# Kernel tuning notes

Measured on AMD Instinct MI355X. Metric: run time of the kernel, lower is better.

Reference implementation:

```python
import jax, jax.numpy as jnp
import numpy as np

N_NODES = 50000
N_EDGES = 800000
IN_DIM = 128
HID = 64
HEADS = 4
OUT_DIM = 20
NUM_GRAPHS = 64
NEG_SLOPE = 0.2  # PyG GATConv default leaky_relu slope


def _xavier(key, shape):
    fan_in, fan_out = shape[-1], shape[0]
    lim = float(np.sqrt(6.0 / (fan_in + fan_out)))
    return jax.random.uniform(key, shape, jnp.float32, -lim, lim)


def setup_inputs() -> dict:
    key = jax.random.key(0)
    ks = jax.random.split(key, 12)
    x = jax.random.normal(ks[0], (N_NODES, IN_DIM), jnp.float32)
    edge_index = jax.random.randint(ks[1], (2, N_EDGES), 0, N_NODES, jnp.int32)
    batch = jnp.sort(jax.random.randint(ks[2], (N_NODES,), 0, NUM_GRAPHS, jnp.int32))
    return {
        "x": x,
        "edge_index": edge_index,
        "batch": batch,
        # conv1: in -> HEADS*HID, concat
        "W1": _xavier(ks[3], (HEADS * HID, IN_DIM)),
        "a_src1": _xavier(ks[4], (HEADS, HID)),
        "a_dst1": _xavier(ks[5], (HEADS, HID)),
        "b1": jnp.zeros((HEADS * HID,), jnp.float32),
        # conv2: HEADS*HID -> HID, 1 head
        "W2": _xavier(ks[6], (HID, HEADS * HID)),
        "a_src2": _xavier(ks[7], (1, HID)),
        "a_dst2": _xavier(ks[8], (1, HID)),
        "b2": jnp.zeros((HID,), jnp.float32),
        "fc_W": _xavier(ks[9], (OUT_DIM, HID)),
        "fc_b": jnp.zeros((OUT_DIM,), jnp.float32),
    }


def _gat_conv(x, src, dst, W, a_src, a_dst, b, heads):
    """PyG GATConv: linear -> per-edge LeakyReLU attention -> softmax over
    incoming edges of each target node -> weighted scatter-sum. Self-loops
    are already included in (src, dst). Dropout omitted (eval mode)."""
    n = x.shape[0]
    h = (x @ W.T).reshape(n, heads, -1)            # [N, H, C]
    alpha_s = jnp.einsum("nhc,hc->nh", h, a_src)   # [N, H]
    alpha_d = jnp.einsum("nhc,hc->nh", h, a_dst)
    e = jax.nn.leaky_relu(alpha_s[src] + alpha_d[dst], NEG_SLOPE)  # [E, H]
    # numerically stable segment softmax over dst
    e_max = jax.ops.segment_max(e, dst, num_segments=n)
    e = jnp.exp(e - e_max[dst])
    denom = jax.ops.segment_sum(e, dst, num_segments=n)
    alpha = e / (denom[dst] + 1e-16)               # [E, H]
    msg = h[src] * alpha[..., None]                # [E, H, C]
    out = jax.ops.segment_sum(msg, dst, num_segments=n)  # [N, H, C]
    return out.reshape(n, -1) + b                  # concat heads


def reference(x, edge_index, batch, W1, a_src1, a_dst1, b1,
              W2, a_src2, a_dst2, b2, fc_W, fc_b):
    n = x.shape[0]
    loops = jnp.arange(n, dtype=edge_index.dtype)
    src = jnp.concatenate([edge_index[0], loops])  # add self-loops (PyG default)
    dst = jnp.concatenate([edge_index[1], loops])
    h = jax.nn.elu(_gat_conv(x, src, dst, W1, a_src1, a_dst1, b1, HEADS))
    h = jax.nn.elu(_gat_conv(h, src, dst, W2, a_src2, a_dst2, b2, 1))
    pooled = jax.ops.segment_max(h, batch, num_segments=NUM_GRAPHS)  # [G, HID]
    return pooled @ fc_W.T + fc_b                  # [G, OUT_DIM]
```

## Files before the change

### kernel.cpp

```cpp
#include <hip/hip_runtime.h>
#include <hip/hip_bf16.h>

#define N_NODES_C 50000
#define N_EDGES_C 800000
#define IN_DIM_C  128
#define HID_C     64
#define HEADS_C   4
#define OUT_DIM_C 20
#define NUM_GRAPHS_C 64
#define NEG_SLOPE 0.2f
#define SCAN_BLOCKS 196

typedef __attribute__((ext_vector_type(8))) short bf16x8;
typedef __attribute__((ext_vector_type(4))) float f32x4;
typedef __attribute__((ext_vector_type(2))) float f32x2;

__device__ __forceinline__ float lrelu(float t){ return t > 0.f ? t : NEG_SLOPE*t; }
__device__ __forceinline__ float elu1(float t){ return t > 0.f ? t : __expf(t)-1.f; }
__device__ __forceinline__ ushort f2bf(float f){
  unsigned u = __float_as_uint(f);
  return (ushort)((u + 0x7fffu + ((u>>16)&1u)) >> 16);
}
__device__ __forceinline__ float bflo(unsigned u){ return __uint_as_float(u<<16); }
__device__ __forceinline__ float bfhi(unsigned u){ return __uint_as_float(u & 0xffff0000u); }
__device__ __forceinline__ float bfs(ushort u){ return __uint_as_float(((unsigned)u)<<16); }

__global__ void hist_kernel(const int* __restrict__ ei, int* __restrict__ cursor){
  int e = blockIdx.x*256 + threadIdx.x;
  if (e < N_EDGES_C) atomicAdd(&cursor[ei[N_EDGES_C + e]], 1);
}

__global__ __launch_bounds__(256) void reduce_counts(const int* __restrict__ cursor, int* __restrict__ blockSums){
  int i = blockIdx.x*256 + threadIdx.x;
  int c = (i < N_NODES_C) ? cursor[i] : 0;
  #pragma unroll
  for(int d=32; d>=1; d>>=1) c += __shfl_xor(c, d);
  __shared__ int s4[4];
  int lane = threadIdx.x & 63, wv = threadIdx.x >> 6;
  if(lane==0) s4[wv] = c;
  __syncthreads();
  if(threadIdx.x==0) blockSums[blockIdx.x] = s4[0]+s4[1]+s4[2]+s4[3];
}

__global__ __launch_bounds__(256) void scan_sums(int* __restrict__ blockSums){
  __shared__ int sh[256];
  int t = threadIdx.x;
  int v = (t < SCAN_BLOCKS) ? blockSums[t] : 0;
  sh[t] = v; __syncthreads();
  #pragma unroll
  for(int off=1; off<256; off<<=1){
    int u = (t>=off) ? sh[t-off] : 0;
    __syncthreads();
    sh[t] += u;
    __syncthreads();
  }
  if(t < SCAN_BLOCKS) blockSums[t] = sh[t] - v;
}

__global__ __launch_bounds__(256) void scan_block(int* __restrict__ cursor, const int* __restrict__ blockSums,
                                                  int* __restrict__ offsets){
  __shared__ int sh[256];
  int t = threadIdx.x;
  int i = blockIdx.x*256 + t;
  int c = (i < N_NODES_C) ? cursor[i] : 0;
  sh[t] = c; __syncthreads();
  #pragma unroll
  for(int off=1; off<256; off<<=1){
    int u = (t>=off) ? sh[t-off] : 0;
    __syncthreads();
    sh[t] += u;
    __syncthreads();
  }
  int excl = sh[t] - c;
  int pref = blockSums[blockIdx.x] + excl;
  if(i < N_NODES_C){
    offsets[i] = pref;
    cursor[i]  = pref;
    if(i == N_NODES_C-1) offsets[N_NODES_C] = pref + c;
  }
}

__global__ void fill_kernel(const int* __restrict__ ei, int* __restrict__ cursor,
                            int* __restrict__ adj, int* __restrict__ dstOf){
  int e = blockIdx.x*256 + threadIdx.x;
  if (e >= N_EDGES_C) return;
  int sI = ei[e]; int d = ei[N_EDGES_C + e];
  int p = atomicAdd(&cursor[d], 1);
  adj[p] = sI;
  dstOf[p] = d;
}

__global__ __launch_bounds__(256) void wperm_kernel(const float* __restrict__ W1, const float* __restrict__ W2,
    ushort* __restrict__ Wp1h, ushort* __restrict__ Wp1l,
    ushort* __restrict__ Wp2h, ushort* __restrict__ Wp2l){
  int i = blockIdx.x*256 + threadIdx.x;
  const float* src; ushort *dh, *dl; int gidx;
  if(i < 4096){
    int kc = i>>10, oc = (i>>6)&15, l = i&63;
    src = W1 + (size_t)(oc*16 + (l&15))*IN_DIM_C + kc*32 + (l>>4)*8;
    dh = Wp1h; dl = Wp1l; gidx = i;
  } else if(i < 4096+2048){
    int i2 = i - 4096;
    int kc = i2>>8, oc = (i2>>6)&3, l = i2&63;
    src = W2 + (size_t)(oc*16 + (l&15))*256 + kc*32 + (l>>4)*8;
    dh = Wp2h; dl = Wp2l; gidx = i2;
  } else return;
  ushort h8[8], l8[8];
  #pragma unroll
  for(int j=0;j<8;j++){
    float f = src[j];
    ushort h = f2bf(f);
    h8[j] = h; l8[j] = f2bf(f - bfs(h));
  }
  #pragma unroll
  for(int j=0;j<8;j++){ dh[gidx*8+j] = h8[j]; dl[gidx*8+j] = l8[j]; }
}

#define HS1_STRIDE 260
__global__ __launch_bounds__(256) void lin1_mfma(const float* __restrict__ x,
    const ushort* __restrict__ Wp1h, const ushort* __restrict__ Wp1l,
    const float* __restrict__ aS, const float* __restrict__ aD,
    ushort* __restrict__ h1, float* __restrict__ as1, float* __restrict__ ad1){
  __shared__ ushort hs[64*HS1_STRIDE];
  int t = threadIdx.x, w = t>>6, l = t&63;
  int n0b = blockIdx.x*64;
  int n0 = n0b + w*16;
  bool active = (n0 < N_NODES_C);
  int row = l & 15, kg = l >> 4;
  if(active){
    bf16x8 ah[4], al[4];
    int gn = n0 + row; if(gn > N_NODES_C-1) gn = N_NODES_C-1;
    const float* xrow = x + (size_t)gn*IN_DIM_C + kg*8;
    #pragma unroll
    for(int kc=0;kc<4;kc++){
      float4 f0 = *(const float4*)(xrow + kc*32);
      float4 f1 = *(const float4*)(xrow + kc*32 + 4);
      float fv[8] = {f0.x,f0.y,f0.z,f0.w,f1.x,f1.y,f1.z,f1.w};
      #pragma unroll
      for(int j=0;j<8;j++){
        ushort h = f2bf(fv[j]);
        float r = fv[j] - bfs(h);
        ah[kc][j] = (short)h;
        al[kc][j] = (short)f2bf(r);
      }
    }
    const bf16x8* Wh = (const bf16x8*)Wp1h + l;
    const bf16x8* Wl = (const bf16x8*)Wp1l + l;
    f32x4 acc[16];
    #pragma unroll
    for(int oc=0;oc<16;oc++){
      f32x4 a = {0.f,0.f,0.f,0.f};
      const bf16x8* ph = Wh + oc*64;
      const bf16x8* pl = Wl + oc*64;
      #pragma unroll
      for(int kc=0;kc<4;kc++){
        bf16x8 bh = ph[kc*1024];
        bf16x8 bl = pl[kc*1024];
        a = __builtin_amdgcn_mfma_f32_16x16x32_bf16(ah[kc], bh, a, 0, 0, 0);
        a = __builtin_amdgcn_mfma_f32_16x16x32_bf16(ah[kc], bl, a, 0, 0, 0);
        a = __builtin_amdgcn_mfma_f32_16x16x32_bf16(al[kc], bh, a, 0, 0, 0);
      }
      acc[oc] = a;
    }
    #pragma unroll
    for(int h=0;h<4;h++){
      float ps0=0.f,ps1=0.f,ps2=0.f,ps3=0.f, pd0=0.f,pd1=0.f,pd2=0.f,pd3=0.f;
      #pragma unroll
      for(int oi=0;oi<4;oi++){
        int oc = h*4 + oi;
        float as_ = aS[oc*16 + row];
        float ad_ = aD[oc*16 + row];
        ps0 = fmaf(acc[oc][0], as_, ps0); pd0 = fmaf(acc[oc][0], ad_, pd0);
        ps1 = fmaf(acc[oc][1], as_, ps1); pd1 = fmaf(acc[oc][1], ad_, pd1);
        ps2 = fmaf(acc[oc][2], as_, ps2); pd2 = fmaf(acc[oc][2], ad_, pd2);
        ps3 = fmaf(acc[oc][3], as_, ps3); pd3 = fmaf(acc[oc][3], ad_, pd3);
      }
      #pragma unroll
      for(int d=1; d<16; d<<=1){
        ps0 += __shfl_xor(ps0,d); ps1 += __shfl_xor(ps1,d);
        ps2 += __shfl_xor(ps2,d); ps3 += __shfl_xor(ps3,d);
        pd0 += __shfl_xor(pd0,d); pd1 += __shfl_xor(pd1,d);
        pd2 += __shfl_xor(pd2,d); pd3 += __shfl_xor(pd3,d);
      }
      if(row==0){
        int nb4 = (n0 + kg*4)*4 + h;
        as1[nb4+0] = ps0; as1[nb4+4] = ps1; as1[nb4+8] = ps2; as1[nb4+12] = ps3;
        ad1[nb4+0] = pd0; ad1[nb4+4] = pd1; ad1[nb4+8] = pd2; ad1[nb4+12] = pd3;
      }
    }
    #pragma unroll
    for(int oc=0;oc<16;oc++){
      #pragma unroll
      for(int r=0;r<4;r++){
        hs[(w*16 + kg*4 + r)*HS1_STRIDE + oc*16 + row] = f2bf(acc[oc][r]);
      }
    }
  }
  __syncthreads();
  int nvalid = N_NODES_C - n0b; if(nvalid > 64) nvalid = 64;
  for(int i=t; i<nvalid*32; i+=256){
    int r = i>>5, c = i&31;
    ((uint4*)(h1 + (size_t)(n0b+r)*256))[c] = *(const uint4*)(hs + r*HS1_STRIDE + c*8);
  }
}

__global__ __launch_bounds__(256) void wexp1_kernel(const int* __restrict__ adj, const int* __restrict__ dstOf,
    const float* __restrict__ as1, const float* __restrict__ ad1, float* __restrict__ wExp){
  int i = blockIdx.x*256 + threadIdx.x;
  if(i >= N_EDGES_C) return;
  int s = adj[i], d = dstOf[i];
  float4 a = ((const float4*)as1)[s];
  float4 b = ((const float4*)ad1)[d];
  float4 w;
  w.x = __expf(lrelu(a.x+b.x));
  w.y = __expf(lrelu(a.y+b.y));
  w.z = __expf(lrelu(a.z+b.z));
  w.w = __expf(lrelu(a.w+b.w));
  ((float4*)wExp)[i] = w;
}

__global__ __launch_bounds__(256) void agg1_kernel(const int* __restrict__ offsets, const int* __restrict__ adj,
    const float* __restrict__ wExp, const ushort* __restrict__ h1,
    const float* __restrict__ as1, const float* __restrict__ ad1,
    const float* __restrict__ b1, float* __restrict__ out1){
  int wv = threadIdx.x>>6, lane = threadIdx.x&63;
  int v = blockIdx.x*4 + wv;
  int head = lane>>4;
  int start = offsets[v], end = offsets[v+1];
  float adh = ad1[(v<<2)+head];
  float ash = as1[(v<<2)+head];
  float wself = __expf(lrelu(ash+adh));
  float denom = wself;
  const char* hb = (const char*)h1;
  unsigned loff = ((unsigned)lane)<<3;
  uint2 pv = *(const uint2*)(hb + ((((unsigned)v)<<9) + loff));
  f32x2 acc01 = {wself*bflo(pv.x), wself*bfhi(pv.x)};
  f32x2 acc23 = {wself*bflo(pv.y), wself*bfhi(pv.y)};
  int i = start;
  for(; i+4 <= end; i += 4){
    int s0 = adj[i], s1 = adj[i+1], s2 = adj[i+2], s3 = adj[i+3];
    float w0 = wExp[(i<<2)+head];
    float w1 = wExp[((i+1)<<2)+head];
    float w2 = wExp[((i+2)<<2)+head];
    float w3 = wExp[((i+3)<<2)+head];
    uint2 p0 = *(const uint2*)(hb + ((((unsigned)s0)<<9) + loff));
    uint2 p1 = *(const uint2*)(hb + ((((unsigned)s1)<<9) + loff));
    uint2 p2 = *(const uint2*)(hb + ((((unsigned)s2)<<9) + loff));
    uint2 p3 = *(const uint2*)(hb + ((((unsigned)s3)<<9) + loff));
    denom += (w0+w1)+(w2+w3);
    f32x2 W0 = {w0,w0}, W1_ = {w1,w1}, W2_ = {w2,w2}, W3_ = {w3,w3};
    f32x2 h0a = {bflo(p0.x), bfhi(p0.x)}, h0b = {bflo(p0.y), bfhi(p0.y)};
    f32x2 h1a = {bflo(p1.x), bfhi(p1.x)}, h1b = {bflo(p1.y), bfhi(p1.y)};
    f32x2 h2a = {bflo(p2.x), bfhi(p2.x)}, h2b = {bflo(p2.y), bfhi(p2.y)};
    f32x2 h3a = {bflo(p3.x), bfhi(p3.x)}, h3b = {bflo(p3.y), bfhi(p3.y)};
    acc01 = __builtin_elementwise_fma(W0, h0a, acc01);
    acc23 = __builtin_elementwise_fma(W0, h0b, acc23);
    acc01 = __builtin_elementwise_fma(W1_, h1a, acc01);
    acc23 = __builtin_elementwise_fma(W1_, h1b, acc23);
    acc01 = __builtin_elementwise_fma(W2_, h2a, acc01);
    acc23 = __builtin_elementwise_fma(W2_, h2b, acc23);
    acc01 = __builtin_elementwise_fma(W3_, h3a, acc01);
    acc23 = __builtin_elementwise_fma(W3_, h3b, acc23);
  }
  for(; i < end; i++){
    int s0 = adj[i];
    float w0 = wExp[(i<<2)+head];
    uint2 p0 = *(const uint2*)(hb + ((((unsigned)s0)<<9) + loff));
    denom += w0;
    f32x2 W0 = {w0,w0};
    f32x2 h0a = {bflo(p0.x), bfhi(p0.x)}, h0b = {bflo(p0.y), bfhi(p0.y)};
    acc01 = __builtin_elementwise_fma(W0, h0a, acc01);
    acc23 = __builtin_elementwise_fma(W0, h0b, acc23);
  }
  float inv = 1.f/(denom + 1e-16f);
  float4 bv = *(const float4*)(b1 + (lane<<2));
  float4 r;
  r.x = elu1(acc01.x*inv + bv.x);
  r.y = elu1(acc01.y*inv + bv.y);
  r.z = elu1(acc23.x*inv + bv.z);
  r.w = elu1(acc23.y*inv + bv.w);
  *(float4*)(out1 + ((size_t)v<<8) + (lane<<2)) = r;
}

#define HS2_STRIDE 68
__global__ __launch_bounds__(256) void lin2_mfma(const float* __restrict__ in,
    const ushort* __restrict__ Wp2h, const ushort* __restrict__ Wp2l,
    const float* __restrict__ aS, const float* __restrict__ aD,
    ushort* __restrict__ h2, float* __restrict__ as2, float* __restrict__ ad2){
  __shared__ ushort hs[64*HS2_STRIDE];
  int t = threadIdx.x, w = t>>6, l = t&63;
  int n0b = blockIdx.x*64;
  int n0 = n0b + w*16;
  bool active = (n0 < N_NODES_C);
  int row = l & 15, kg = l >> 4;
  if(active){
    bf16x8 ah[8], al[8];
    int gn = n0 + row; if(gn > N_NODES_C-1) gn = N_NODES_C-1;
    const float* xrow = in + (size_t)gn*256 + kg*8;
    #pragma unroll
    for(int kc=0;kc<8;kc++){
      float4 f0 = *(const float4*)(xrow + kc*32);
      float4 f1 = *(const float4*)(xrow + kc*32 + 4);
      float fv[8] = {f0.x,f0.y,f0.z,f0.w,f1.x,f1.y,f1.z,f1.w};
      #pragma unroll
      for(int j=0;j<8;j++){
        ushort h = f2bf(fv[j]);
        float r = fv[j] - bfs(h);
        ah[kc][j] = (short)h;
        al[kc][j] = (short)f2bf(r);
      }
    }
    const bf16x8* Wh = (const bf16x8*)Wp2h + l;
    const bf16x8* Wl = (const bf16x8*)Wp2l + l;
    f32x4 acc[4];
    #pragma unroll
    for(int oc=0;oc<4;oc++){
      f32x4 a = {0.f,0.f,0.f,0.f};
      const bf16x8* ph = Wh + oc*64;
      const bf16x8* pl = Wl + oc*64;
      #pragma unroll
      for(int kc=0;kc<8;kc++){
        bf16x8 bh = ph[kc*256];
        bf16x8 bl = pl[kc*256];
        a = __builtin_amdgcn_mfma_f32_16x16x32_bf16(ah[kc], bh, a, 0, 0, 0);
        a = __builtin_amdgcn_mfma_f32_16x16x32_bf16(ah[kc], bl, a, 0, 0, 0);
        a = __builtin_amdgcn_mfma_f32_16x16x32_bf16(al[kc], bh, a, 0, 0, 0);
      }
      acc[oc] = a;
    }
    {
      float ps0=0.f,ps1=0.f,ps2=0.f,ps3=0.f, pd0=0.f,pd1=0.f,pd2=0.f,pd3=0.f;
      #pragma unroll
      for(int oc=0;oc<4;oc++){
        float as_ = aS[oc*16 + row];
        float ad_ = aD[oc*16 + row];
        ps0 = fmaf(acc[oc][0], as_, ps0); pd0 = fmaf(acc[oc][0], ad_, pd0);
        ps1 = fmaf(acc[oc][1], as_, ps1); pd1 = fmaf(acc[oc][1], ad_, pd1);
        ps2 = fmaf(acc[oc][2], as_, ps2); pd2 = fmaf(acc[oc][2], ad_, pd2);
        ps3 = fmaf(acc[oc][3], as_, ps3); pd3 = fmaf(acc[oc][3], ad_, pd3);
      }
      #pragma unroll
      for(int d=1; d<16; d<<=1){
        ps0 += __shfl_xor(ps0,d); ps1 += __shfl_xor(ps1,d);
        ps2 += __shfl_xor(ps2,d); ps3 += __shfl_xor(ps3,d);
        pd0 += __shfl_xor(pd0,d); pd1 += __shfl_xor(pd1,d);
        pd2 += __shfl_xor(pd2,d); pd3 += __shfl_xor(pd3,d);
      }
      if(row==0){
        int n = n0 + kg*4;
        as2[n+0] = ps0; as2[n+1] = ps1; as2[n+2] = ps2; as2[n+3] = ps3;
        ad2[n+0] = pd0; ad2[n+1] = pd1; ad2[n+2] = pd2; ad2[n+3] = pd3;
      }
    }
    #pragma unroll
    for(int oc=0;oc<4;oc++){
      #pragma unroll
      for(int r=0;r<4;r++){
        hs[(w*16 + kg*4 + r)*HS2_STRIDE + oc*16 + row] = f2bf(acc[oc][r]);
      }
    }
  }
  __syncthreads();
  int nvalid = N_NODES_C - n0b; if(nvalid > 64) nvalid = 64;
  for(int i=t; i<nvalid*8; i+=256){
    int r = i>>3, c = i&7;
    ((uint4*)(h2 + (size_t)(n0b+r)*64))[c] = *(const uint4*)(hs + r*HS2_STRIDE + c*8);
  }
}

__global__ __launch_bounds__(256) void wexp2_kernel(const int* __restrict__ adj, const int* __restrict__ dstOf,
    const float* __restrict__ as2, const float* __restrict__ ad2, float* __restrict__ wExp2){
  int i = blockIdx.x*256 + threadIdx.x;
  if(i >= N_EDGES_C) return;
  int s = adj[i], d = dstOf[i];
  wExp2[i] = __expf(lrelu(as2[s] + ad2[d]));
}

__global__ __launch_bounds__(256) void agg2_kernel(const int* __restrict__ offsets, const int* __restrict__ adj,
    const float* __restrict__ wExp2, const ushort* __restrict__ h2,
    const float* __restrict__ as2, const float* __restrict__ ad2,
    const float* __restrict__ b2, float* __restrict__ out2){
  int wv = threadIdx.x>>6, lane = threadIdx.x&63;
  int v = blockIdx.x*4 + wv;
  int half = lane>>5, sl = lane&31;
  int start = offsets[v], end = offsets[v+1];
  float adv = ad2[v], asv = as2[v];
  float wself = __expf(lrelu(asv+adv));
  const unsigned* hu = (const unsigned*)h2;
  float denom = half ? 0.f : wself;
  f32x2 acc = {0.f, 0.f};
  if(!half){
    unsigned us = hu[(((unsigned)v)<<5) + sl];
    acc.x = wself*bflo(us); acc.y = wself*bfhi(us);
  }
  for(int i=start+half; i<end; i+=2){
    int s = adj[i];
    float wg = wExp2[i];
    unsigned u = hu[(((unsigned)s)<<5) + sl];
    denom += wg;
    f32x2 Wp = {wg, wg};
    f32x2 hp = {bflo(u), bfhi(u)};
    acc = __builtin_elementwise_fma(Wp, hp, acc);
  }
  acc.x += __shfl_xor(acc.x, 32);
  acc.y += __shfl_xor(acc.y, 32);
  denom += __shfl_xor(denom, 32);
  if(!half){
    float inv = 1.f/(denom + 1e-16f);
    float2 bv = *(const float2*)(b2 + sl*2);
    float2 r;
    r.x = elu1(acc.x*inv + bv.x);
    r.y = elu1(acc.y*inv + bv.y);
    *(float2*)(out2 + (((size_t)v)<<6) + sl*2) = r;
  }
}

__global__ __launch_bounds__(256) void pool_fc_kernel(const float* __restrict__ out2, const int* __restrict__ batch,
    const float* __restrict__ fcW, const float* __restrict__ fcb, float* __restrict__ out){
  int g = blockIdx.x;
  int tid=threadIdx.x; int c = tid&63; int slot = tid>>6;
  int lo=0, hi=N_NODES_C;
  while(lo<hi){ int mid=(lo+hi)>>1; if(batch[mid] < g) lo=mid+1; else hi=mid; }
  int start=lo;
  hi=N_NODES_C;
  while(lo<hi){ int mid=(lo+hi)>>1; if(batch[mid] < g+1) lo=mid+1; else hi=mid; }
  int end=lo;
  float mm = -INFINITY;
  #pragma unroll 4
  for(int n=start+slot; n<end; n+=4) mm = fmaxf(mm, out2[(size_t)n*64+c]);
  __shared__ float sred[4][64];
  sred[slot][c]=mm;
  __syncthreads();
  if(tid < 64){
    float p = fmaxf(fmaxf(sred[0][tid],sred[1][tid]), fmaxf(sred[2][tid],sred[3][tid]));
    sred[0][tid]=p;
  }
  __syncthreads();
  if(tid < OUT_DIM_C){
    float acc = fcb[tid];
    #pragma unroll
    for(int cc=0;cc<64;cc++) acc = fmaf(sred[0][cc], fcW[tid*64+cc], acc);
    out[g*OUT_DIM_C + tid] = acc;
  }
}

extern "C" void kernel_launch(void* const* d_in, const int* in_sizes, int n_in,
                              void* d_out, int out_size, void* d_ws, size_t ws_size,
                              hipStream_t stream) {
  const float* x   = (const float*)d_in[0];
  const int*   ei  = (const int*)  d_in[1];
  const int*   bat = (const int*)  d_in[2];
  const float* W1  = (const float*)d_in[3];
  const float* aS1 = (const float*)d_in[4];
  const float* aD1 = (const float*)d_in[5];
  const float* b1  = (const float*)d_in[6];
  const float* W2  = (const float*)d_in[7];
  const float* aS2 = (const float*)d_in[8];
  const float* aD2 = (const float*)d_in[9];
  const float* b2  = (const float*)d_in[10];
  const float* fcW = (const float*)d_in[11];
  const float* fcb = (const float*)d_in[12];
  float* out = (float*)d_out;

  char* w = (char*)d_ws;
  size_t off = 0;
  auto alloc = [&](size_t bytes)->char* {
    char* p = w + off; off = (off + bytes + 255) & ~(size_t)255; return p;
  };
  int* offsets   = (int*)alloc((N_NODES_C+1)*sizeof(int));
  int* cursor    = (int*)alloc((size_t)N_NODES_C*sizeof(int));
  int* blockSums = (int*)alloc(SCAN_BLOCKS*sizeof(int));
  int* adj       = (int*)alloc((size_t)(N_EDGES_C+4)*sizeof(int));
  int* dstOf     = (int*)alloc((size_t)N_EDGES_C*sizeof(int));
  ushort* Wp1h   = (ushort*)alloc((size_t)4096*8*sizeof(ushort));
  ushort* Wp1l   = (ushort*)alloc((size_t)4096*8*sizeof(ushort));
  ushort* Wp2h   = (ushort*)alloc((size_t)2048*8*sizeof(ushort));
  ushort* Wp2l   = (ushort*)alloc((size_t)2048*8*sizeof(ushort));
  ushort* h1     = (ushort*)alloc((size_t)N_NODES_C*256*sizeof(ushort));
  float* as1     = (float*)alloc((size_t)N_NODES_C*4*sizeof(float));
  float* ad1     = (float*)alloc((size_t)N_NODES_C*4*sizeof(float));
  float* out1    = (float*)alloc((size_t)N_NODES_C*256*sizeof(float));
  float* wExp    = (float*)alloc(((size_t)N_EDGES_C*4+4)*sizeof(float));
  ushort* h2  = h1;
  float* as2  = as1;
  float* ad2  = ad1;
  float* out2 = out1;
  float* wExp2 = wExp;
  (void)ws_size; (void)in_sizes; (void)n_in; (void)out_size;

  hipMemsetAsync(cursor, 0, (size_t)N_NODES_C*sizeof(int), stream);
  hist_kernel<<<(N_EDGES_C+255)/256, 256, 0, stream>>>(ei, cursor);
  reduce_counts<<<SCAN_BLOCKS, 256, 0, stream>>>(cursor, blockSums);
  scan_sums<<<1, 256, 0, stream>>>(blockSums);
  scan_block<<<SCAN_BLOCKS, 256, 0, stream>>>(cursor, blockSums, offsets);
  fill_kernel<<<(N_EDGES_C+255)/256, 256, 0, stream>>>(ei, cursor, adj, dstOf);
  wperm_kernel<<<24, 256, 0, stream>>>(W1, W2, Wp1h, Wp1l, Wp2h, Wp2l);

  lin1_mfma<<<(N_NODES_C+63)/64, 256, 0, stream>>>(x, Wp1h, Wp1l, aS1, aD1, h1, as1, ad1);
  wexp1_kernel<<<(N_EDGES_C+255)/256, 256, 0, stream>>>(adj, dstOf, as1, ad1, wExp);
  agg1_kernel<<<N_NODES_C/4, 256, 0, stream>>>(offsets, adj, wExp, h1, as1, ad1, b1, out1);
  lin2_mfma<<<(N_NODES_C+63)/64, 256, 0, stream>>>(out1, Wp2h, Wp2l, aS2, aD2, h2, as2, ad2);
  wexp2_kernel<<<(N_EDGES_C+255)/256, 256, 0, stream>>>(adj, dstOf, as2, ad2, wExp2);
  agg2_kernel<<<N_NODES_C/4, 256, 0, stream>>>(offsets, adj, wExp2, h2, as2, ad2, b2, out2);
  pool_fc_kernel<<<NUM_GRAPHS_C, 256, 0, stream>>>(out2, bat, fcW, fcb, out);
}
```

Baseline: 421.0 us.

## Fuse edge attention weight computation into aggregation kernels, drop dstOf and wExp buffers

Removes the separate wexp1/wexp2 kernels and the dstOf array. Each aggregation kernel now gathers the source attention score and computes exp(leakyrelu) inline, since the destination score is already in a register. This cuts two launches, the dstOf write in fill, and the write-then-read of the per-edge weight buffer. The agg1 loop is unrolled to 8 edges and agg2 to 2 per half-wave, adding more independent gathers per iteration. The cost is extra exp math and random as1 gathers, with each lane of a head group recomputing the same weight.

```diff
diff --git a/kernel.cpp b/kernel.cpp
--- a/kernel.cpp
+++ b/kernel.cpp
@@ -81,13 +81,12 @@
 }
 
 __global__ void fill_kernel(const int* __restrict__ ei, int* __restrict__ cursor,
-                            int* __restrict__ adj, int* __restrict__ dstOf){
+                            int* __restrict__ adj){
   int e = blockIdx.x*256 + threadIdx.x;
   if (e >= N_EDGES_C) return;
   int sI = ei[e]; int d = ei[N_EDGES_C + e];
   int p = atomicAdd(&cursor[d], 1);
   adj[p] = sI;
-  dstOf[p] = d;
 }
 
 __global__ __launch_bounds__(256) void wperm_kernel(const float* __restrict__ W1, const float* __restrict__ W2,
@@ -204,23 +203,8 @@
   }
 }
 
-__global__ __launch_bounds__(256) void wexp1_kernel(const int* __restrict__ adj, const int* __restrict__ dstOf,
-    const float* __restrict__ as1, const float* __restrict__ ad1, float* __restrict__ wExp){
-  int i = blockIdx.x*256 + threadIdx.x;
-  if(i >= N_EDGES_C) return;
-  int s = adj[i], d = dstOf[i];
-  float4 a = ((const float4*)as1)[s];
-  float4 b = ((const float4*)ad1)[d];
-  float4 w;
-  w.x = __expf(lrelu(a.x+b.x));
-  w.y = __expf(lrelu(a.y+b.y));
-  w.z = __expf(lrelu(a.z+b.z));
-  w.w = __expf(lrelu(a.w+b.w));
-  ((float4*)wExp)[i] = w;
-}
-
 __global__ __launch_bounds__(256) void agg1_kernel(const int* __restrict__ offsets, const int* __restrict__ adj,
-    const float* __restrict__ wExp, const ushort* __restrict__ h1,
+    const ushort* __restrict__ h1,
     const float* __restrict__ as1, const float* __restrict__ ad1,
     const float* __restrict__ b1, float* __restrict__ out1){
   int wv = threadIdx.x>>6, lane = threadIdx.x&63;
@@ -237,40 +221,61 @@
   f32x2 acc01 = {wself*bflo(pv.x), wself*bfhi(pv.x)};
   f32x2 acc23 = {wself*bflo(pv.y), wself*bfhi(pv.y)};
   int i = start;
-  for(; i+4 <= end; i += 4){
-    int s0 = adj[i], s1 = adj[i+1], s2 = adj[i+2], s3 = adj[i+3];
-    float w0 = wExp[(i<<2)+head];
-    float w1 = wExp[((i+1)<<2)+head];
-    float w2 = wExp[((i+2)<<2)+head];
-    float w3 = wExp[((i+3)<<2)+head];
+  for(; i+8 <= end; i += 8){
+    int s0 = adj[i],   s1 = adj[i+1], s2 = adj[i+2], s3 = adj[i+3];
+    int s4 = adj[i+4], s5 = adj[i+5], s6 = adj[i+6], s7 = adj[i+7];
+    float a0 = as1[(s0<<2)+head], a1 = as1[(s1<<2)+head];
+    float a2 = as1[(s2<<2)+head], a3 = as1[(s3<<2)+head];
+    float a4 = as1[(s4<<2)+head], a5 = as1[(s5<<2)+head];
+    float a6 = as1[(s6<<2)+head], a7 = as1[(s7<<2)+head];
     uint2 p0 = *(const uint2*)(hb + ((((unsigned)s0)<<9) + loff));
     uint2 p1 = *(const uint2*)(hb + ((((unsigned)s1)<<9) + loff));
     uint2 p2 = *(const uint2*)(hb + ((((unsigned)s2)<<9) + loff));
     uint2 p3 = *(const uint2*)(hb + ((((unsigned)s3)<<9) + loff));
-    denom += (w0+w1)+(w2+w3);
-    f32x2 W0 = {w0,w0}, W1_ = {w1,w1}, W2_ = {w2,w2}, W3_ = {w3,w3};
-    f32x2 h0a = {bflo(p0.x), bfhi(p0.x)}, h0b = {bflo(p0.y), bfhi(p0.y)};
-    f32x2 h1a = {bflo(p1.x), bfhi(p1.x)}, h1b = {bflo(p1.y), bfhi(p1.y)};
-    f32x2 h2a = {bflo(p2.x), bfhi(p2.x)}, h2b = {bflo(p2.y), bfhi(p2.y)};
-    f32x2 h3a = {bflo(p3.x), bfhi(p3.x)}, h3b = {bflo(p3.y), bfhi(p3.y)};
-    acc01 = __builtin_elementwise_fma(W0, h0a, acc01);
-    acc23 = __builtin_elementwise_fma(W0, h0b, acc23);
-    acc01 = __builtin_elementwise_fma(W1_, h1a, acc01);
-    acc23 = __builtin_elementwise_fma(W1_, h1b, acc23);
-    acc01 = __builtin_elementwise_fma(W2_, h2a, acc01);
-    acc23 = __builtin_elementwise_fma(W2_, h2b, acc23);
-    acc01 = __builtin_elementwise_fma(W3_, h3a, acc01);
-    acc23 = __builtin_elementwise_fma(W3_, h3b, acc23);
+    uint2 p4 = *(const uint2*)(hb + ((((unsigned)s4)<<9) + loff));
+    uint2 p5 = *(const uint2*)(hb + ((((unsigned)s5)<<9) + loff));
+    uint2 p6 = *(const uint2*)(hb + ((((unsigned)s6)<<9) + loff));
+    uint2 p7 = *(const uint2*)(hb + ((((unsigned)s7)<<9) + loff));
+    float w0 = __expf(lrelu(a0+adh)), w1 = __expf(lrelu(a1+adh));
+    float w2 = __expf(lrelu(a2+adh)), w3 = __expf(lrelu(a3+adh));
+    float w4 = __expf(lrelu(a4+adh)), w5 = __expf(lrelu(a5+adh));
+    float w6 = __expf(lrelu(a6+adh)), w7 = __expf(lrelu(a7+adh));
+    denom += ((w0+w1)+(w2+w3)) + ((w4+w5)+(w6+w7));
+    f32x2 W;
+    W.x = w0; W.y = w0;
+    acc01 = __builtin_elementwise_fma(W, (f32x2){bflo(p0.x), bfhi(p0.x)}, acc01);
+    acc23 = __builtin_elementwise_fma(W, (f32x2){bflo(p0.y), bfhi(p0.y)}, acc23);
+    W.x = w1; W.y = w1;
+    acc01 = __builtin_elementwise_fma(W, (f32x2){bflo(p1.x), bfhi(p1.x)}, acc01);
+    acc23 = __builtin_elementwise_fma(W, (f32x2){bflo(p1.y), bfhi(p1.y)}, acc23);
+    W.x = w2; W.y = w2;
+    acc01 = __builtin_elementwise_fma(W, (f32x2){bflo(p2.x), bfhi(p2.x)}, acc01);
+    acc23 = __builtin_elementwise_fma(W, (f32x2){bflo(p2.y), bfhi(p2.y)}, acc23);
+    W.x = w3; W.y = w3;
+    acc01 = __builtin_elementwise_fma(W, (f32x2){bflo(p3.x), bfhi(p3.x)}, acc01);
+    acc23 = __builtin_elementwise_fma(W, (f32x2){bflo(p3.y), bfhi(p3.y)}, acc23);
+    W.x = w4; W.y = w4;
+    acc01 = __builtin_elementwise_fma(W, (f32x2){bflo(p4.x), bfhi(p4.x)}, acc01);
+    acc23 = __builtin_elementwise_fma(W, (f32x2){bflo(p4.y), bfhi(p4.y)}, acc23);
+    W.x = w5; W.y = w5;
+    acc01 = __builtin_elementwise_fma(W, (f32x2){bflo(p5.x), bfhi(p5.x)}, acc01);
+    acc23 = __builtin_elementwise_fma(W, (f32x2){bflo(p5.y), bfhi(p5.y)}, acc23);
+    W.x = w6; W.y = w6;
+    acc01 = __builtin_elementwise_fma(W, (f32x2){bflo(p6.x), bfhi(p6.x)}, acc01);
+    acc23 = __builtin_elementwise_fma(W, (f32x2){bflo(p6.y), bfhi(p6.y)}, acc23);
+    W.x = w7; W.y = w7;
+    acc01 = __builtin_elementwise_fma(W, (f32x2){bflo(p7.x), bfhi(p7.x)}, acc01);
+    acc23 = __builtin_elementwise_fma(W, (f32x2){bflo(p7.y), bfhi(p7.y)}, acc23);
   }
   for(; i < end; i++){
     int s0 = adj[i];
-    float w0 = wExp[(i<<2)+head];
+    float a0 = as1[(s0<<2)+head];
     uint2 p0 = *(const uint2*)(hb + ((((unsigned)s0)<<9) + loff));
+    float w0 = __expf(lrelu(a0+adh));
     denom += w0;
-    f32x2 W0 = {w0,w0};
-    f32x2 h0a = {bflo(p0.x), bfhi(p0.x)}, h0b = {bflo(p0.y), bfhi(p0.y)};
-    acc01 = __builtin_elementwise_fma(W0, h0a, acc01);
-    acc23 = __builtin_elementwise_fma(W0, h0b, acc23);
+    f32x2 W; W.x = w0; W.y = w0;
+    acc01 = __builtin_elementwise_fma(W, (f32x2){bflo(p0.x), bfhi(p0.x)}, acc01);
+    acc23 = __builtin_elementwise_fma(W, (f32x2){bflo(p0.y), bfhi(p0.y)}, acc23);
   }
   float inv = 1.f/(denom + 1e-16f);
   float4 bv = *(const float4*)(b1 + (lane<<2));
@@ -368,16 +373,8 @@
   }
 }
 
-__global__ __launch_bounds__(256) void wexp2_kernel(const int* __restrict__ adj, const int* __restrict__ dstOf,
-    const float* __restrict__ as2, const float* __restrict__ ad2, float* __restrict__ wExp2){
-  int i = blockIdx.x*256 + threadIdx.x;
-  if(i >= N_EDGES_C) return;
-  int s = adj[i], d = dstOf[i];
-  wExp2[i] = __expf(lrelu(as2[s] + ad2[d]));
-}
-
 __global__ __launch_bounds__(256) void agg2_kernel(const int* __restrict__ offsets, const int* __restrict__ adj,
-    const float* __restrict__ wExp2, const ushort* __restrict__ h2,
+    const ushort* __restrict__ h2,
     const float* __restrict__ as2, const float* __restrict__ ad2,
     const float* __restrict__ b2, float* __restrict__ out2){
   int wv = threadIdx.x>>6, lane = threadIdx.x&63;
@@ -393,14 +390,28 @@
     unsigned us = hu[(((unsigned)v)<<5) + sl];
     acc.x = wself*bflo(us); acc.y = wself*bfhi(us);
   }
-  for(int i=start+half; i<end; i+=2){
+  int i = start + half;
+  for(; i+2 < end; i += 4){
+    int sA = adj[i], sB = adj[i+2];
+    float aA = as2[sA], aB = as2[sB];
+    unsigned uA = hu[(((unsigned)sA)<<5) + sl];
+    unsigned uB = hu[(((unsigned)sB)<<5) + sl];
+    float wA = __expf(lrelu(aA+adv));
+    float wB = __expf(lrelu(aB+adv));
+    denom += wA + wB;
+    f32x2 W;
+    W.x = wA; W.y = wA;
+    acc = __builtin_elementwise_fma(W, (f32x2){bflo(uA), bfhi(uA)}, acc);
+    W.x = wB; W.y = wB;
+    acc = __builtin_elementwise_fma(W, (f32x2){bflo(uB), bfhi(uB)}, acc);
+  }
+  for(; i < end; i += 2){
     int s = adj[i];
-    float wg = wExp2[i];
+    float wg = __expf(lrelu(as2[s]+adv));
     unsigned u = hu[(((unsigned)s)<<5) + sl];
     denom += wg;
-    f32x2 Wp = {wg, wg};
-    f32x2 hp = {bflo(u), bfhi(u)};
-    acc = __builtin_elementwise_fma(Wp, hp, acc);
+    f32x2 W; W.x = wg; W.y = wg;
+    acc = __builtin_elementwise_fma(W, (f32x2){bflo(u), bfhi(u)}, acc);
   }
   acc.x += __shfl_xor(acc.x, 32);
   acc.y += __shfl_xor(acc.y, 32);
@@ -470,8 +481,7 @@
   int* offsets   = (int*)alloc((N_NODES_C+1)*sizeof(int));
   int* cursor    = (int*)alloc((size_t)N_NODES_C*sizeof(int));
   int* blockSums = (int*)alloc(SCAN_BLOCKS*sizeof(int));
-  int* adj       = (int*)alloc((size_t)(N_EDGES_C+4)*sizeof(int));
-  int* dstOf     = (int*)alloc((size_t)N_EDGES_C*sizeof(int));
+  int* adj       = (int*)alloc((size_t)(N_EDGES_C+8)*sizeof(int));
   ushort* Wp1h   = (ushort*)alloc((size_t)4096*8*sizeof(ushort));
   ushort* Wp1l   = (ushort*)alloc((size_t)4096*8*sizeof(ushort));
   ushort* Wp2h   = (ushort*)alloc((size_t)2048*8*sizeof(ushort));
@@ -480,12 +490,10 @@
   float* as1     = (float*)alloc((size_t)N_NODES_C*4*sizeof(float));
   float* ad1     = (float*)alloc((size_t)N_NODES_C*4*sizeof(float));
   float* out1    = (float*)alloc((size_t)N_NODES_C*256*sizeof(float));
-  float* wExp    = (float*)alloc(((size_t)N_EDGES_C*4+4)*sizeof(float));
   ushort* h2  = h1;
   float* as2  = as1;
   float* ad2  = ad1;
   float* out2 = out1;
-  float* wExp2 = wExp;
   (void)ws_size; (void)in_sizes; (void)n_in; (void)out_size;
 
   hipMemsetAsync(cursor, 0, (size_t)N_NODES_C*sizeof(int), stream);
@@ -493,14 +501,12 @@
   reduce_counts<<<SCAN_BLOCKS, 256, 0, stream>>>(cursor, blockSums);
   scan_sums<<<1, 256, 0, stream>>>(blockSums);
   scan_block<<<SCAN_BLOCKS, 256, 0, stream>>>(cursor, blockSums, offsets);
-  fill_kernel<<<(N_EDGES_C+255)/256, 256, 0, stream>>>(ei, cursor, adj, dstOf);
+  fill_kernel<<<(N_EDGES_C+255)/256, 256, 0, stream>>>(ei, cursor, adj);
   wperm_kernel<<<24, 256, 0, stream>>>(W1, W2, Wp1h, Wp1l, Wp2h, Wp2l);
 
   lin1_mfma<<<(N_NODES_C+63)/64, 256, 0, stream>>>(x, Wp1h, Wp1l, aS1, aD1, h1, as1, ad1);
-  wexp1_kernel<<<(N_EDGES_C+255)/256, 256, 0, stream>>>(adj, dstOf, as1, ad1, wExp);
-  agg1_kernel<<<N_NODES_C/4, 256, 0, stream>>>(offsets, adj, wExp, h1, as1, ad1, b1, out1);
+  agg1_kernel<<<N_NODES_C/4, 256, 0, stream>>>(offsets, adj, h1, as1, ad1, b1, out1);
   lin2_mfma<<<(N_NODES_C+63)/64, 256, 0, stream>>>(out1, Wp2h, Wp2l, aS2, aD2, h2, as2, ad2);
-  wexp2_kernel<<<(N_EDGES_C+255)/256, 256, 0, stream>>>(adj, dstOf, as2, ad2, wExp2);
-  agg2_kernel<<<N_NODES_C/4, 256, 0, stream>>>(offsets, adj, wExp2, h2, as2, ad2, b2, out2);
+  agg2_kernel<<<N_NODES_C/4, 256, 0, stream>>>(offsets, adj, h2, as2, ad2, b2, out2);
   pool_fc_kernel<<<NUM_GRAPHS_C, 256, 0, stream>>>(out2, bat, fcW, fcb, out);
 }
```

Result: faster. 395.1 us (-6.2%).
